# Optimization experiments

Hardware: AMD Instinct MI355X
Metric: run time of the kernel (lower is better)

The kernel has to match this reference:

```python
import jax, jax.numpy as jnp
import numpy as np

B, S, V, D, H, L, FF = 2, 1024, 32000, 512, 8, 4, 2048
DK = D // H
WIN, GLOB = 128, 16
EPS = 1e-5


def setup_inputs() -> dict:
    key = jax.random.key(0)
    ks = jax.random.split(key, 12)
    def rn(k, shape, s=0.02):
        return jax.random.normal(k, shape, jnp.float32) * s
    ln2 = jnp.stack([jnp.ones((L, 2, D)), jnp.zeros((L, 2, D))], axis=2)   # [L, 2 norms, (scale,bias), D]
    ln3 = jnp.stack([jnp.ones((L, 3, D)), jnp.zeros((L, 3, D))], axis=2)   # [L, 3 norms, (scale,bias), D]
    fln = jnp.stack([jnp.ones((D,)), jnp.zeros((D,))], axis=0)             # [(scale,bias), D]
    return {
        "src": jax.random.randint(ks[0], (B, S), 0, V),
        "tgt": jax.random.randint(ks[1], (B, S), 0, V),
        "enc_embed": rn(ks[2], (V, D)),
        "dec_embed": rn(ks[3], (V, D)),
        "enc_attn_w": rn(ks[4], (L, 4, D, D)),   # q,k,v,o projections
        "enc_attn_b": jnp.zeros((L, 4, D)),
        "enc_ln": ln2,
        "enc_ffn_w1": rn(ks[5], (L, D, FF)),
        "enc_ffn_b1": jnp.zeros((L, FF)),
        "enc_ffn_w2": rn(ks[6], (L, FF, D)),
        "enc_ffn_b2": jnp.zeros((L, D)),
        "enc_final_ln": fln,
        "dec_attn_w": rn(ks[7], (L, 8, D, D)),   # self q,k,v,o then cross q,k,v,o
        "dec_attn_b": jnp.zeros((L, 8, D)),
        "dec_ln": ln3,
        "dec_ffn_w1": rn(ks[8], (L, D, FF)),
        "dec_ffn_b1": jnp.zeros((L, FF)),
        "dec_ffn_w2": rn(ks[9], (L, FF, D)),
        "dec_ffn_b2": jnp.zeros((L, D)),
        "dec_final_ln": fln,
        "out_w": rn(ks[10], (D, V)),
        "out_b": jnp.zeros((V,)),
    }


def _ln(x, p):
    m = jnp.mean(x, -1, keepdims=True)
    v = jnp.var(x, -1, keepdims=True)
    return p[0] * (x - m) * jax.lax.rsqrt(v + EPS) + p[1]


def _rope(x):
    # x: [B, H, S, DK]; half-split rotary embedding
    half = DK // 2
    pos = jnp.arange(x.shape[2], dtype=jnp.float32)
    inv = 1.0 / (10000.0 ** (jnp.arange(half, dtype=jnp.float32) / half))
    ang = pos[:, None] * inv[None, :]                   # [S, half]
    c, s = jnp.cos(ang), jnp.sin(ang)
    x1, x2 = x[..., :half], x[..., half:]
    return jnp.concatenate([x1 * c - x2 * s, x1 * s + x2 * c], axis=-1)


def _mask(n, causal):
    # local sliding window + global tokens, optional causal
    i = jnp.arange(n)[:, None]
    j = jnp.arange(n)[None, :]
    allowed = jnp.abs(i - j) <= WIN
    allowed = allowed | (i < GLOB) | (j < GLOB)
    if causal:
        allowed = allowed & (j <= i)
    return allowed


def _attn(q_in, k_in, v_in, w, b, causal):
    # w: [4, D, D] (q,k,v,o), b: [4, D]
    def heads(x, idx):
        y = x @ w[idx] + b[idx]
        return y.reshape(x.shape[0], x.shape[1], H, DK).transpose(0, 2, 1, 3)  # [B,H,S,DK]
    Q, K, Vh = heads(q_in, 0), heads(k_in, 1), heads(v_in, 2)
    Q, K = _rope(Q), _rope(K)
    scores = jnp.einsum('bhqd,bhkd->bhqk', Q, K) / np.sqrt(DK).astype(np.float32)
    scores = jnp.where(_mask(q_in.shape[1], causal)[None, None], scores, -1e9)
    A = jax.nn.softmax(scores, axis=-1)
    o = jnp.einsum('bhqk,bhkd->bhqd', A, Vh).transpose(0, 2, 1, 3).reshape(q_in.shape[0], q_in.shape[1], D)
    return o @ w[3] + b[3]


def _ffn(x, w1, b1, w2, b2):
    return jax.nn.gelu(x @ w1 + b1) @ w2 + b2


def _forward(src, tgt, enc_embed, dec_embed, enc_attn_w, enc_attn_b, enc_ln,
             enc_ffn_w1, enc_ffn_b1, enc_ffn_w2, enc_ffn_b2, enc_final_ln,
             dec_attn_w, dec_attn_b, dec_ln, dec_ffn_w1, dec_ffn_b1,
             dec_ffn_w2, dec_ffn_b2, dec_final_ln, out_w, out_b):
    sqrt_d = np.sqrt(D).astype(np.float32)
    # encoder
    x = enc_embed[src] * sqrt_d
    for l in range(L):
        n = _ln(x, enc_ln[l, 0])
        x = x + _attn(n, n, n, enc_attn_w[l], enc_attn_b[l], False)
        n = _ln(x, enc_ln[l, 1])
        x = x + _ffn(n, enc_ffn_w1[l], enc_ffn_b1[l], enc_ffn_w2[l], enc_ffn_b2[l])
    mem = _ln(x, enc_final_ln)
    # decoder
    y = dec_embed[tgt] * sqrt_d
    for l in range(L):
        n = _ln(y, dec_ln[l, 0])
        y = y + _attn(n, n, n, dec_attn_w[l, :4], dec_attn_b[l, :4], True)
        n = _ln(y, dec_ln[l, 1])
        y = y + _attn(n, mem, mem, dec_attn_w[l, 4:], dec_attn_b[l, 4:], False)
        n = _ln(y, dec_ln[l, 2])
        y = y + _ffn(n, dec_ffn_w1[l], dec_ffn_b1[l], dec_ffn_w2[l], dec_ffn_b2[l])
    y = _ln(y, dec_final_ln)
    return y @ out_w + out_b


def reference(src, tgt, enc_embed, dec_embed, enc_attn_w, enc_attn_b, enc_ln,
              enc_ffn_w1, enc_ffn_b1, enc_ffn_w2, enc_ffn_b2, enc_final_ln,
              dec_attn_w, dec_attn_b, dec_ln, dec_ffn_w1, dec_ffn_b1,
              dec_ffn_w2, dec_ffn_b2, dec_final_ln, out_w, out_b):
    return _forward(src, tgt, enc_embed, dec_embed, enc_attn_w, enc_attn_b, enc_ln,
                    enc_ffn_w1, enc_ffn_b1, enc_ffn_w2, enc_ffn_b2, enc_final_ln,
                    dec_attn_w, dec_attn_b, dec_ln, dec_ffn_w1, dec_ffn_b1,
                    dec_ffn_w2, dec_ffn_b2, dec_final_ln, out_w, out_b)
```

## Files before the change

kernel.cpp:

```cpp
#include <hip/hip_runtime.h>
#include <cstdint>
#include <cstddef>

#define S_LEN 1024
#define DM 512
#define NHEAD 8
#define HDIM 64
#define NLAYER 4
#define FFD 2048
#define VOC 32000
#define WINSZ 128
#define GLOBSZ 16

using half8 = __attribute__((ext_vector_type(8))) _Float16;
using f32x4 = __attribute__((ext_vector_type(4))) float;

static __device__ __forceinline__ f32x4 mfma16(half8 a, half8 b, f32x4 c) {
  return __builtin_amdgcn_mfma_f32_16x16x32_f16(a, b, c, 0, 0, 0);
}

typedef __attribute__((address_space(1))) const void gvoid;
typedef __attribute__((address_space(3))) void lvoid;
static __device__ __forceinline__ void gload16(const void* g, void* l) {
  __builtin_amdgcn_global_load_lds((gvoid*)g, (lvoid*)l, 16, 0, 0);
}
template <int N>
static __device__ __forceinline__ void waitv() {
  asm volatile("s_waitcnt vmcnt(%0)" :: "i"(N) : "memory");
}

__global__ __launch_bounds__(256) void transpose_k(const float* __restrict__ in,
                                                   _Float16* __restrict__ out,
                                                   int R, int C)
{
  __shared__ float t[32][33];
  const float* ip = in + (size_t)blockIdx.z * R * C;
  _Float16* op = out + (size_t)blockIdx.z * R * C;
  int c0 = blockIdx.x * 32, r0 = blockIdx.y * 32;
  int tx = threadIdx.x & 31, ty = threadIdx.x >> 5;
#pragma unroll
  for (int i = 0; i < 32; i += 8)
    t[ty + i][tx] = ip[(size_t)(r0 + ty + i) * C + c0 + tx];
  __syncthreads();
#pragma unroll
  for (int i = 0; i < 32; i += 8)
    op[(size_t)(c0 + ty + i) * R + r0 + tx] = (_Float16)t[tx][ty + i];
}

__global__ __launch_bounds__(256) void embed2_k(const int* __restrict__ src,
                                                const int* __restrict__ tgt,
                                                const float* __restrict__ enc_embed,
                                                const float* __restrict__ dec_embed,
                                                const float* __restrict__ enc_ln0,
                                                const float* __restrict__ dec_ln0,
                                                float* __restrict__ xbuf,
                                                float* __restrict__ ybuf,
                                                _Float16* __restrict__ nbuf,
                                                _Float16* __restrict__ nbuf2)
{
  int which = blockIdx.y;
  const int* ids = which ? tgt : src;
  const float* emb = which ? dec_embed : enc_embed;
  const float* gamma = which ? dec_ln0 : enc_ln0;
  const float* beta = gamma + 512;
  float* xout = which ? ybuf : xbuf;
  _Float16* nout = which ? nbuf2 : nbuf;

  int row = blockIdx.x * 4 + (threadIdx.x >> 6);
  int lane = threadIdx.x & 63;
  const float* er = emb + (size_t)ids[row] * DM + lane * 8;
  float4 v0 = *(const float4*)er;
  float4 v1 = *(const float4*)(er + 4);
  float vals[8] = {v0.x, v0.y, v0.z, v0.w, v1.x, v1.y, v1.z, v1.w};
  float s = 0.f, ss = 0.f;
#pragma unroll
  for (int j = 0; j < 8; ++j) {
    vals[j] *= 22.627416997969522f;
    s += vals[j]; ss += vals[j] * vals[j];
  }
#pragma unroll
  for (int m = 1; m < 64; m <<= 1) { s += __shfl_xor(s, m); ss += __shfl_xor(ss, m); }
  float mean = s * (1.f / 512.f);
  float var = ss * (1.f / 512.f) - mean * mean;
  float rstd = rsqrtf(var + 1e-5f);
  float* xr = xout + (size_t)row * DM + lane * 8;
  _Float16* orow = nout + (size_t)row * DM + lane * 8;
  const float* gp = gamma + lane * 8;
  const float* bp = beta + lane * 8;
#pragma unroll
  for (int j = 0; j < 8; ++j) {
    xr[j] = vals[j];
    orow[j] = (_Float16)(gp[j] * (vals[j] - mean) * rstd + bp[j]);
  }
}

__global__ __launch_bounds__(256) void ln_k(const float* __restrict__ x,
                                            const float* __restrict__ gamma,
                                            const float* __restrict__ beta,
                                            _Float16* __restrict__ outp)
{
  int row = blockIdx.x * 4 + (threadIdx.x >> 6);
  int lane = threadIdx.x & 63;
  const float* xr = x + (size_t)row * DM + lane * 8;
  float4 v0 = *(const float4*)xr;
  float4 v1 = *(const float4*)(xr + 4);
  float vals[8] = {v0.x, v0.y, v0.z, v0.w, v1.x, v1.y, v1.z, v1.w};
  float s = 0.f, ss = 0.f;
#pragma unroll
  for (int j = 0; j < 8; ++j) { s += vals[j]; ss += vals[j] * vals[j]; }
#pragma unroll
  for (int m = 1; m < 64; m <<= 1) { s += __shfl_xor(s, m); ss += __shfl_xor(ss, m); }
  float mean = s * (1.f / 512.f);
  float var = ss * (1.f / 512.f) - mean * mean;
  float rstd = rsqrtf(var + 1e-5f);
  _Float16* orow = outp + (size_t)row * DM + lane * 8;
  const float* gp = gamma + lane * 8;
  const float* bp = beta + lane * 8;
#pragma unroll
  for (int j = 0; j < 8; ++j)
    orow[j] = (_Float16)(gp[j] * (vals[j] - mean) * rstd + bp[j]);
}

template <int BM, int BN, int EPI, int MODE>
__global__ __launch_bounds__(256) void gemm_k(const _Float16* __restrict__ A,
                                              const _Float16* __restrict__ B,
                                              const float* __restrict__ bias,
                                              const float* __restrict__ resid,
                                              void* __restrict__ Cout,
                                              _Float16* __restrict__ vtout,
                                              int M, int N, int K)
{
  constexpr bool WIDE = (BN >= 64);
  constexpr int WAVE_M = WIDE ? BM / 4 : BM / 2;
  constexpr int FMW = WAVE_M / 16;
  constexpr int FNW = WIDE ? BN / 16 : BN / 32;
  constexpr int LPS = BM / 32 + BN / 32;
  static_assert(MODE == 0 || (WIDE && BN == 64), "rope modes need 64-col waves");

  __shared__ __align__(16) _Float16 As[3][BM * 64];
  __shared__ __align__(16) _Float16 Bs[3][BN * 64];
  const int tid = threadIdx.x;
  const int lane = tid & 63, wid = tid >> 6;
  const int g = lane >> 4, ql = lane & 15;
  const int bm = blockIdx.x * BM, bn = blockIdx.y * BN;
  const int wm = WIDE ? wid * WAVE_M : (wid >> 1) * WAVE_M;
  const int wn = WIDE ? 0 : (wid & 1) * (BN / 2);

  const _Float16* Bp;
  if constexpr (MODE == 2) {
    int srcrow0 = ((bn >> 10) * 8 + 5 + ((bn >> 9) & 1)) * 512 + (bn & 511);
    Bp = B + (size_t)srcrow0 * K;
  } else {
    Bp = B + (size_t)bn * K;
  }

  f32x4 acc[FMW][FNW];
#pragma unroll
  for (int a = 0; a < FMW; ++a)
#pragma unroll
    for (int b = 0; b < FNW; ++b) acc[a][b] = f32x4{0.f, 0.f, 0.f, 0.f};

  auto stage = [&](int buf, int kt) {
#pragma unroll
    for (int r = 0; r < BM / 32; ++r) {
      int off = r * 4096 + tid * 16;
      int row = off >> 7, slot = (off >> 4) & 7;
      gload16(A + (size_t)(bm + row) * K + kt + ((slot ^ (row & 7)) << 3),
              (char*)&As[buf][0] + r * 4096 + wid * 1024);
    }
#pragma unroll
    for (int r = 0; r < BN / 32; ++r) {
      int off = r * 4096 + tid * 16;
      int row = off >> 7, slot = (off >> 4) & 7;
      gload16(Bp + (size_t)row * K + kt + ((slot ^ (row & 7)) << 3),
              (char*)&Bs[buf][0] + r * 4096 + wid * 1024);
    }
  };

  auto compute = [&](int cur) {
#pragma unroll
    for (int kk = 0; kk < 2; ++kk) {
      half8 af[FMW], bf[FNW];
#pragma unroll
      for (int a = 0; a < FMW; ++a) {
        int row = wm + a * 16 + ql;
        af[a] = *(const half8*)((const char*)&As[cur][0] + row * 128 + (((kk * 4 + g) ^ (row & 7)) << 4));
      }
#pragma unroll
      for (int b = 0; b < FNW; ++b) {
        int row = wn + b * 16 + ql;
        bf[b] = *(const half8*)((const char*)&Bs[cur][0] + row * 128 + (((kk * 4 + g) ^ (row & 7)) << 4));
      }
#pragma unroll
      for (int a = 0; a < FMW; ++a)
#pragma unroll
        for (int b = 0; b < FNW; ++b) acc[a][b] = mfma16(af[a], bf[b], acc[a][b]);
    }
  };

  const int nk = K >> 6;
  stage(0, 0);
  stage(1, 64);
  for (int t = 0; t < nk; ++t) {
    if (t + 1 < nk) waitv<LPS>(); else waitv<0>();
    __builtin_amdgcn_s_barrier();
    __builtin_amdgcn_sched_barrier(0);
    compute(t % 3);
    if (t + 2 < nk) stage((t + 2) % 3, (t + 2) << 6);
  }

#pragma unroll
  for (int a = 0; a < FMW; ++a) {
    const int row0 = bm + wm + a * 16 + g * 4;
    float v[FNW][4];
#pragma unroll
    for (int b2 = 0; b2 < FNW; ++b2) {
      int col = bn + wn + b2 * 16 + ql;
      float bv;
      if constexpr (MODE == 2) {
        int bcol = ((col >> 10) * 8 + 5 + ((col >> 9) & 1)) * 512 + (col & 511);
        bv = bias[bcol];
      } else {
        bv = bias[col];
      }
#pragma unroll
      for (int r = 0; r < 4; ++r) v[b2][r] = acc[a][b2][r] + bv;
    }
    if constexpr (MODE != 0) {
      const int seg = bn >> 9;
      bool dorope = (MODE == 3) || (MODE == 1 && seg < 2) ||
                    (MODE == 2 && ((bn >> 9) & 1) == 0);
      if (dorope) {
        const float scale = (MODE == 3 || (MODE == 1 && seg == 0)) ? 0.125f : 1.0f;
#pragma unroll
        for (int b2 = 0; b2 < 2; ++b2) {
          int d = b2 * 16 + ql;
          float inv = __expf(-(float)d * 0.28782313662425574f);
#pragma unroll
          for (int r = 0; r < 4; ++r) {
            float sp = (float)((row0 & 1023) + r);
            float sn, cs; __sincosf(sp * inv, &sn, &cs);
            float x1 = v[b2][r], x2 = v[b2 + 2][r];
            v[b2][r]     = (x1 * cs - x2 * sn) * scale;
            v[b2 + 2][r] = (x1 * sn + x2 * cs) * scale;
          }
        }
      }
    }
#pragma unroll
    for (int b2 = 0; b2 < FNW; ++b2) {
      int col = bn + wn + b2 * 16 + ql;
      if constexpr (MODE == 1) {
        if (col < 1024) {
#pragma unroll
          for (int r = 0; r < 4; ++r)
            ((_Float16*)Cout)[(size_t)(row0 + r) * 1024 + col] = (_Float16)v[b2][r];
        } else {
          int rowidx = ((row0 >> 10) << 9) + (col - 1024);
          union { _Float16 h[4]; uint2 u; } pk;
#pragma unroll
          for (int r = 0; r < 4; ++r) pk.h[r] = (_Float16)v[b2][r];
          *(uint2*)&vtout[((size_t)rowidx << 10) + (row0 & 1023)] = pk.u;
        }
      } else if constexpr (MODE == 2) {
        if ((col & 1023) < 512) {
#pragma unroll
          for (int r = 0; r < 4; ++r)
            ((_Float16*)Cout)[(size_t)(row0 + r) * 2048 + ((col >> 10) << 9) + (col & 511)] = (_Float16)v[b2][r];
        } else {
          int rowidx = (col & ~1023) + ((row0 >> 10) << 9) + (col & 511);
          union { _Float16 h[4]; uint2 u; } pk;
#pragma unroll
          for (int r = 0; r < 4; ++r) pk.h[r] = (_Float16)v[b2][r];
          *(uint2*)&vtout[((size_t)rowidx << 10) + (row0 & 1023)] = pk.u;
        }
      } else {
#pragma unroll
        for (int r = 0; r < 4; ++r) {
          float x = v[b2][r];
          if constexpr (EPI == 1) {
            float u = x;
            x = u / (1.f + __expf(-1.5957691216057308f * (u + 0.044715f * u * u * u)));
          }
          if constexpr (EPI == 2) x += resid[(size_t)(row0 + r) * N + col];
          if constexpr (EPI == 0 || EPI == 1)
            ((_Float16*)Cout)[(size_t)(row0 + r) * N + col] = (_Float16)x;
          else
            ((float*)Cout)[(size_t)(row0 + r) * N + col] = x;
        }
      }
    }
  }
}

template <bool CAUSAL>
__global__ __launch_bounds__(256) void attn_k(const _Float16* __restrict__ qb, int qs, int qoff,
                                              const _Float16* __restrict__ kb, int ks, int koff,
                                              const _Float16* __restrict__ vt,
                                              _Float16* __restrict__ out)
{
  __shared__ _Float16 plds[4][16 * 40];
  const int bh = blockIdx.y, b = bh >> 3, h = bh & 7;
  const int wid = threadIdx.x >> 6, lane = threadIdx.x & 63;
  const int g = lane >> 4, ql = lane & 15;
  const int q0 = blockIdx.x * 64 + wid * 16;
  const size_t rb = (size_t)b * S_LEN;

  half8 qf0, qf1;
  {
    const _Float16* qp = qb + (rb + q0 + ql) * qs + qoff + h * HDIM + g * 8;
    qf0 = *(const half8*)qp;
    qf1 = *(const half8*)(qp + 32);
  }
  float mrun[4] = {-1e30f, -1e30f, -1e30f, -1e30f};
  float srun[4] = {0.f, 0.f, 0.f, 0.f};
  f32x4 oacc[4];
#pragma unroll
  for (int c = 0; c < 4; ++c) oacc[c] = f32x4{0.f, 0.f, 0.f, 0.f};

  const _Float16* vbase = vt + (((size_t)(b * 512 + h * HDIM)) << 10);
  _Float16* pw = plds[wid];

  auto proc = [&](int k0) {
    const _Float16* kp = kb + (rb + k0 + ql) * ks + koff + h * HDIM + g * 8;
    half8 kf00 = *(const half8*)kp;
    half8 kf01 = *(const half8*)(kp + 32);
    half8 kf10 = *(const half8*)(kp + (size_t)16 * ks);
    half8 kf11 = *(const half8*)(kp + (size_t)16 * ks + 32);

    f32x4 s0 = f32x4{0.f, 0.f, 0.f, 0.f};
    f32x4 s1 = f32x4{0.f, 0.f, 0.f, 0.f};
    s0 = mfma16(qf0, kf00, s0); s0 = mfma16(qf1, kf01, s0);
    s1 = mfma16(qf0, kf10, s1); s1 = mfma16(qf1, kf11, s1);

    float p0[4], p1[4];
#pragma unroll
    for (int r = 0; r < 4; ++r) {
      int i = q0 + 4 * g + r;
      int j0 = k0 + ql, j1 = j0 + 16;
      float a0 = s0[r], a1 = s1[r];
      int d0 = i - j0, d1 = i - j1;
      bool ok0 = (d0 <= WINSZ && d0 >= -WINSZ) || (i < GLOBSZ) || (j0 < GLOBSZ);
      bool ok1 = (d1 <= WINSZ && d1 >= -WINSZ) || (i < GLOBSZ) || (j1 < GLOBSZ);
      if (CAUSAL) { ok0 = ok0 && (j0 <= i); ok1 = ok1 && (j1 <= i); }
      a0 = ok0 ? a0 : -1e9f;
      a1 = ok1 ? a1 : -1e9f;
      float mx = fmaxf(a0, a1);
      mx = fmaxf(mx, __shfl_xor(mx, 1));
      mx = fmaxf(mx, __shfl_xor(mx, 2));
      mx = fmaxf(mx, __shfl_xor(mx, 4));
      mx = fmaxf(mx, __shfl_xor(mx, 8));
      float mnew = fmaxf(mrun[r], mx);
      float alpha = __expf(mrun[r] - mnew);
      float e0 = __expf(a0 - mnew), e1 = __expf(a1 - mnew);
      float ps = e0 + e1;
      ps += __shfl_xor(ps, 1);
      ps += __shfl_xor(ps, 2);
      ps += __shfl_xor(ps, 4);
      ps += __shfl_xor(ps, 8);
      srun[r] = srun[r] * alpha + ps;
      mrun[r] = mnew;
#pragma unroll
      for (int c = 0; c < 4; ++c) oacc[c][r] *= alpha;
      p0[r] = e0; p1[r] = e1;
    }
#pragma unroll
    for (int r = 0; r < 4; ++r) {
      pw[(4 * g + r) * 40 + ql] = (_Float16)p0[r];
      pw[(4 * g + r) * 40 + 16 + ql] = (_Float16)p1[r];
    }
    half8 pa = *(const half8*)&pw[ql * 40 + g * 8];
#pragma unroll
    for (int c = 0; c < 4; ++c) {
      half8 vf = *(const half8*)(vbase + (((size_t)(16 * c + ql)) << 10) + k0 + 8 * g);
      oacc[c] = mfma16(pa, vf, oacc[c]);
    }
  };

  const int kend = CAUSAL ? (q0 + 16) : S_LEN;
  int lo = 0, hi = kend;
  if (q0 >= GLOBSZ) {
    lo = (q0 - WINSZ) & ~31;
    if (lo < 0) lo = 0;
    if (!CAUSAL) {
      int h2 = q0 + 16 + WINSZ;
      hi = (h2 < kend) ? h2 : kend;
    }
  }
  if (lo > 0) proc(0);
  for (int k0 = lo; k0 < hi; k0 += 32) proc(k0);

#pragma unroll
  for (int c = 0; c < 4; ++c)
#pragma unroll
    for (int r = 0; r < 4; ++r) {
      float val = oacc[c][r] / srun[r];
      out[(rb + q0 + 4 * g + r) * DM + h * HDIM + 16 * c + ql] = (_Float16)val;
    }
}

extern "C" void kernel_launch(void* const* d_in, const int* in_sizes, int n_in,
                              void* d_out, int out_size, void* d_ws, size_t ws_size,
                              hipStream_t stream)
{
  const int*   src         = (const int*)d_in[0];
  const int*   tgt         = (const int*)d_in[1];
  const float* enc_embed   = (const float*)d_in[2];
  const float* dec_embed   = (const float*)d_in[3];
  const float* enc_attn_w  = (const float*)d_in[4];
  const float* enc_attn_b  = (const float*)d_in[5];
  const float* enc_ln      = (const float*)d_in[6];
  const float* enc_ffn_w1  = (const float*)d_in[7];
  const float* enc_ffn_b1  = (const float*)d_in[8];
  const float* enc_ffn_w2  = (const float*)d_in[9];
  const float* enc_ffn_b2  = (const float*)d_in[10];
  const float* enc_fln     = (const float*)d_in[11];
  const float* dec_attn_w  = (const float*)d_in[12];
  const float* dec_attn_b  = (const float*)d_in[13];
  const float* dec_ln      = (const float*)d_in[14];
  const float* dec_ffn_w1  = (const float*)d_in[15];
  const float* dec_ffn_b1  = (const float*)d_in[16];
  const float* dec_ffn_w2  = (const float*)d_in[17];
  const float* dec_ffn_b2  = (const float*)d_in[18];
  const float* dec_fln     = (const float*)d_in[19];
  const float* out_w       = (const float*)d_in[20];
  const float* out_b       = (const float*)d_in[21];
  float* logits = (float*)d_out;

  char* wsp = (char*)d_ws;
  size_t off = 0;
  auto alloc = [&](size_t bytes) -> void* {
    void* p = wsp + off;
    off += (bytes + 255) & ~(size_t)255;
    return p;
  };
  _Float16* enc_attn_wt = (_Float16*)alloc((size_t)16 * 512 * 512 * 2);
  _Float16* dec_attn_wt = (_Float16*)alloc((size_t)32 * 512 * 512 * 2);
  _Float16* e_ffn1_wt   = (_Float16*)alloc((size_t)4 * 2048 * 512 * 2);
  _Float16* e_ffn2_wt   = (_Float16*)alloc((size_t)4 * 2048 * 512 * 2);
  _Float16* d_ffn1_wt   = (_Float16*)alloc((size_t)4 * 2048 * 512 * 2);
  _Float16* d_ffn2_wt   = (_Float16*)alloc((size_t)4 * 2048 * 512 * 2);
  _Float16* out_wt      = (_Float16*)alloc((size_t)VOC * 512 * 2);
  float*    xbuf        = (float*)alloc((size_t)2048 * 512 * 4);
  float*    ybuf        = (float*)alloc((size_t)2048 * 512 * 4);
  _Float16* nbuf        = (_Float16*)alloc((size_t)2048 * 512 * 2);
  _Float16* nbuf2       = (_Float16*)alloc((size_t)2048 * 512 * 2);
  _Float16* qkvb        = (_Float16*)alloc((size_t)2048 * 1024 * 2);
  _Float16* aob         = (_Float16*)alloc((size_t)2048 * 512 * 2);
  _Float16* hbuf        = (_Float16*)alloc((size_t)2048 * 2048 * 2);
  _Float16* memb        = (_Float16*)alloc((size_t)2048 * 512 * 2);
  _Float16* cqb         = (_Float16*)alloc((size_t)2048 * 512 * 2);
  _Float16* ckvb        = (_Float16*)alloc((size_t)2048 * 2048 * 2);
  _Float16* vts         = (_Float16*)alloc((size_t)2 * 512 * 1024 * 2);
  _Float16* vtc         = (_Float16*)alloc((size_t)8 * 512 * 1024 * 2);

  transpose_k<<<dim3(16, 16, 16), 256, 0, stream>>>(enc_attn_w, enc_attn_wt, 512, 512);
  transpose_k<<<dim3(16, 16, 32), 256, 0, stream>>>(dec_attn_w, dec_attn_wt, 512, 512);
  transpose_k<<<dim3(64, 16, 4), 256, 0, stream>>>(enc_ffn_w1, e_ffn1_wt, 512, 2048);
  transpose_k<<<dim3(16, 64, 4), 256, 0, stream>>>(enc_ffn_w2, e_ffn2_wt, 2048, 512);
  transpose_k<<<dim3(64, 16, 4), 256, 0, stream>>>(dec_ffn_w1, d_ffn1_wt, 512, 2048);
  transpose_k<<<dim3(16, 64, 4), 256, 0, stream>>>(dec_ffn_w2, d_ffn2_wt, 2048, 512);
  transpose_k<<<dim3(1000, 16, 1), 256, 0, stream>>>(out_w, out_wt, 512, VOC);

  embed2_k<<<dim3(512, 2), 256, 0, stream>>>(src, tgt, enc_embed, dec_embed,
                                             enc_ln, dec_ln, xbuf, ybuf, nbuf, nbuf2);

  for (int l = 0; l < NLAYER; ++l) {
    const float* g0 = enc_ln + ((size_t)(l * 2 + 0) * 2 + 0) * 512;
    if (l > 0) ln_k<<<512, 256, 0, stream>>>(xbuf, g0, g0 + 512, nbuf);
    gemm_k<64, 64, 0, 1><<<dim3(32, 24), 256, 0, stream>>>(
        nbuf, enc_attn_wt + (size_t)l * 4 * 262144,
        enc_attn_b + (size_t)l * 4 * 512, nullptr, qkvb, vts, 2048, 1536, 512);
    attn_k<false><<<dim3(16, 16), 256, 0, stream>>>(qkvb, 1024, 0, qkvb, 1024, 512, vts, aob);
    gemm_k<64, 32, 2, 0><<<dim3(32, 16), 256, 0, stream>>>(
        aob, enc_attn_wt + (size_t)(l * 4 + 3) * 262144,
        enc_attn_b + (size_t)(l * 4 + 3) * 512, xbuf, xbuf, nullptr, 2048, 512, 512);
    const float* g1 = enc_ln + ((size_t)(l * 2 + 1) * 2 + 0) * 512;
    ln_k<<<512, 256, 0, stream>>>(xbuf, g1, g1 + 512, nbuf);
    gemm_k<64, 64, 1, 0><<<dim3(32, 32), 256, 0, stream>>>(
        nbuf, e_ffn1_wt + (size_t)l * 2048 * 512,
        enc_ffn_b1 + (size_t)l * 2048, nullptr, hbuf, nullptr, 2048, 2048, 512);
    gemm_k<64, 32, 2, 0><<<dim3(32, 16), 256, 0, stream>>>(
        hbuf, e_ffn2_wt + (size_t)l * 512 * 2048,
        enc_ffn_b2 + (size_t)l * 512, xbuf, xbuf, nullptr, 2048, 512, 2048);
  }
  ln_k<<<512, 256, 0, stream>>>(xbuf, enc_fln, enc_fln + 512, memb);

  gemm_k<64, 64, 0, 2><<<dim3(32, 64), 256, 0, stream>>>(
      memb, dec_attn_wt, dec_attn_b, nullptr, ckvb, vtc, 2048, 4096, 512);

  for (int l = 0; l < NLAYER; ++l) {
    const float* g0 = dec_ln + ((size_t)(l * 3 + 0) * 2 + 0) * 512;
    const _Float16* dn = (l == 0) ? nbuf2 : nbuf;
    if (l > 0) ln_k<<<512, 256, 0, stream>>>(ybuf, g0, g0 + 512, nbuf);
    gemm_k<64, 64, 0, 1><<<dim3(32, 24), 256, 0, stream>>>(
        dn, dec_attn_wt + (size_t)l * 8 * 262144,
        dec_attn_b + (size_t)l * 8 * 512, nullptr, qkvb, vts, 2048, 1536, 512);
    attn_k<true><<<dim3(16, 16), 256, 0, stream>>>(qkvb, 1024, 0, qkvb, 1024, 512, vts, aob);
    gemm_k<64, 32, 2, 0><<<dim3(32, 16), 256, 0, stream>>>(
        aob, dec_attn_wt + (size_t)(l * 8 + 3) * 262144,
        dec_attn_b + (size_t)(l * 8 + 3) * 512, ybuf, ybuf, nullptr, 2048, 512, 512);
    const float* g1 = dec_ln + ((size_t)(l * 3 + 1) * 2 + 0) * 512;
    ln_k<<<512, 256, 0, stream>>>(ybuf, g1, g1 + 512, nbuf);
    gemm_k<64, 64, 0, 3><<<dim3(32, 8), 256, 0, stream>>>(
        nbuf, dec_attn_wt + (size_t)(l * 8 + 4) * 262144,
        dec_attn_b + (size_t)(l * 8 + 4) * 512, nullptr, cqb, nullptr, 2048, 512, 512);
    attn_k<false><<<dim3(16, 16), 256, 0, stream>>>(cqb, 512, 0, ckvb, 2048, l * 512,
                                                    vtc + ((size_t)l << 20), aob);
    gemm_k<64, 32, 2, 0><<<dim3(32, 16), 256, 0, stream>>>(
        aob, dec_attn_wt + (size_t)(l * 8 + 7) * 262144,
        dec_attn_b + (size_t)(l * 8 + 7) * 512, ybuf, ybuf, nullptr, 2048, 512, 512);
    const float* g2 = dec_ln + ((size_t)(l * 3 + 2) * 2 + 0) * 512;
    ln_k<<<512, 256, 0, stream>>>(ybuf, g2, g2 + 512, nbuf);
    gemm_k<64, 64, 1, 0><<<dim3(32, 32), 256, 0, stream>>>(
        nbuf, d_ffn1_wt + (size_t)l * 2048 * 512,
        dec_ffn_b1 + (size_t)l * 2048, nullptr, hbuf, nullptr, 2048, 2048, 512);
    gemm_k<64, 32, 2, 0><<<dim3(32, 16), 256, 0, stream>>>(
        hbuf, d_ffn2_wt + (size_t)l * 512 * 2048,
        dec_ffn_b2 + (size_t)l * 512, ybuf, ybuf, nullptr, 2048, 512, 2048);
  }

  ln_k<<<512, 256, 0, stream>>>(ybuf, dec_fln, dec_fln + 512, nbuf);
  gemm_k<128, 64, 3, 0><<<dim3(16, 500), 256, 0, stream>>>(
      nbuf, out_wt, out_b, nullptr, logits, nullptr, 2048, VOC, 512);
}
```

Before: 1.061 ms.

## Remap GEMM blocks across XCDs, prefetch before compute, widen residual tiles

The GEMM kernel remaps its linear block id so that consecutive tiles land on the same XCD chiplet, which is meant to improve L2 reuse of shared A/B panels. The next-stage global-to-LDS load is now issued before the MFMA compute instead of after it, to overlap more. The residual GEMMs move from 64x32 tiles (512 blocks) to 64x64 tiles (256 blocks), dropping the narrow-wave path. The logits output uses nontemporal stores. These trade fewer blocks (less parallelism on 256 CUs) and a possible LDS hazard from issuing the load early against better reuse and overlap.

```diff
diff --git a/kernel.cpp b/kernel.cpp
--- a/kernel.cpp
+++ b/kernel.cpp
@@ -130,21 +130,26 @@
                                               _Float16* __restrict__ vtout,
                                               int M, int N, int K)
 {
-  constexpr bool WIDE = (BN >= 64);
-  constexpr int WAVE_M = WIDE ? BM / 4 : BM / 2;
+  constexpr int WAVE_M = BM / 4;
   constexpr int FMW = WAVE_M / 16;
-  constexpr int FNW = WIDE ? BN / 16 : BN / 32;
+  constexpr int FNW = BN / 16;
   constexpr int LPS = BM / 32 + BN / 32;
-  static_assert(MODE == 0 || (WIDE && BN == 64), "rope modes need 64-col waves");
+  static_assert(BN == 64 || MODE == 0, "rope modes need 64-col waves");
 
   __shared__ __align__(16) _Float16 As[3][BM * 64];
   __shared__ __align__(16) _Float16 Bs[3][BN * 64];
   const int tid = threadIdx.x;
   const int lane = tid & 63, wid = tid >> 6;
   const int g = lane >> 4, ql = lane & 15;
-  const int bm = blockIdx.x * BM, bn = blockIdx.y * BN;
-  const int wm = WIDE ? wid * WAVE_M : (wid >> 1) * WAVE_M;
-  const int wn = WIDE ? 0 : (wid & 1) * (BN / 2);
+
+  const int gx = gridDim.x;
+  const int nwg = gx * gridDim.y;
+  const int orig = blockIdx.y * gx + blockIdx.x;
+  const int q = nwg >> 3, r = nwg & 7;
+  const int xcd = orig & 7, rest = orig >> 3;
+  const int id = (xcd < r ? xcd * (q + 1) : r * (q + 1) + (xcd - r) * q) + rest;
+  const int bm = (id % gx) * BM, bn = (id / gx) * BN;
+  const int wm = wid * WAVE_M, wn = 0;
 
   const _Float16* Bp;
   if constexpr (MODE == 2) {
@@ -162,18 +167,18 @@
 
   auto stage = [&](int buf, int kt) {
 #pragma unroll
-    for (int r = 0; r < BM / 32; ++r) {
-      int off = r * 4096 + tid * 16;
+    for (int r2 = 0; r2 < BM / 32; ++r2) {
+      int off = r2 * 4096 + tid * 16;
       int row = off >> 7, slot = (off >> 4) & 7;
       gload16(A + (size_t)(bm + row) * K + kt + ((slot ^ (row & 7)) << 3),
-              (char*)&As[buf][0] + r * 4096 + wid * 1024);
-    }
-#pragma unroll
-    for (int r = 0; r < BN / 32; ++r) {
-      int off = r * 4096 + tid * 16;
+              (char*)&As[buf][0] + r2 * 4096 + wid * 1024);
+    }
+#pragma unroll
+    for (int r2 = 0; r2 < BN / 32; ++r2) {
+      int off = r2 * 4096 + tid * 16;
       int row = off >> 7, slot = (off >> 4) & 7;
       gload16(Bp + (size_t)row * K + kt + ((slot ^ (row & 7)) << 3),
-              (char*)&Bs[buf][0] + r * 4096 + wid * 1024);
+              (char*)&Bs[buf][0] + r2 * 4096 + wid * 1024);
     }
   };
 
@@ -205,8 +210,8 @@
     if (t + 1 < nk) waitv<LPS>(); else waitv<0>();
     __builtin_amdgcn_s_barrier();
     __builtin_amdgcn_sched_barrier(0);
+    if (t + 2 < nk) stage((t + 2) % 3, (t + 2) << 6);
     compute(t % 3);
-    if (t + 2 < nk) stage((t + 2) % 3, (t + 2) << 6);
   }
 
 #pragma unroll
@@ -224,7 +229,7 @@
         bv = bias[col];
       }
 #pragma unroll
-      for (int r = 0; r < 4; ++r) v[b2][r] = acc[a][b2][r] + bv;
+      for (int r2 = 0; r2 < 4; ++r2) v[b2][r2] = acc[a][b2][r2] + bv;
     }
     if constexpr (MODE != 0) {
       const int seg = bn >> 9;
@@ -237,12 +242,12 @@
           int d = b2 * 16 + ql;
           float inv = __expf(-(float)d * 0.28782313662425574f);
 #pragma unroll
-          for (int r = 0; r < 4; ++r) {
-            float sp = (float)((row0 & 1023) + r);
+          for (int r2 = 0; r2 < 4; ++r2) {
+            float sp = (float)((row0 & 1023) + r2);
             float sn, cs; __sincosf(sp * inv, &sn, &cs);
-            float x1 = v[b2][r], x2 = v[b2 + 2][r];
-            v[b2][r]     = (x1 * cs - x2 * sn) * scale;
-            v[b2 + 2][r] = (x1 * sn + x2 * cs) * scale;
+            float x1 = v[b2][r2], x2 = v[b2 + 2][r2];
+            v[b2][r2]     = (x1 * cs - x2 * sn) * scale;
+            v[b2 + 2][r2] = (x1 * sn + x2 * cs) * scale;
           }
         }
       }
@@ -253,40 +258,42 @@
       if constexpr (MODE == 1) {
         if (col < 1024) {
 #pragma unroll
-          for (int r = 0; r < 4; ++r)
-            ((_Float16*)Cout)[(size_t)(row0 + r) * 1024 + col] = (_Float16)v[b2][r];
+          for (int r2 = 0; r2 < 4; ++r2)
+            ((_Float16*)Cout)[(size_t)(row0 + r2) * 1024 + col] = (_Float16)v[b2][r2];
         } else {
           int rowidx = ((row0 >> 10) << 9) + (col - 1024);
           union { _Float16 h[4]; uint2 u; } pk;
 #pragma unroll
-          for (int r = 0; r < 4; ++r) pk.h[r] = (_Float16)v[b2][r];
+          for (int r2 = 0; r2 < 4; ++r2) pk.h[r2] = (_Float16)v[b2][r2];
           *(uint2*)&vtout[((size_t)rowidx << 10) + (row0 & 1023)] = pk.u;
         }
       } else if constexpr (MODE == 2) {
         if ((col & 1023) < 512) {
 #pragma unroll
-          for (int r = 0; r < 4; ++r)
-            ((_Float16*)Cout)[(size_t)(row0 + r) * 2048 + ((col >> 10) << 9) + (col & 511)] = (_Float16)v[b2][r];
+          for (int r2 = 0; r2 < 4; ++r2)
+            ((_Float16*)Cout)[(size_t)(row0 + r2) * 2048 + ((col >> 10) << 9) + (col & 511)] = (_Float16)v[b2][r2];
         } else {
           int rowidx = (col & ~1023) + ((row0 >> 10) << 9) + (col & 511);
           union { _Float16 h[4]; uint2 u; } pk;
 #pragma unroll
-          for (int r = 0; r < 4; ++r) pk.h[r] = (_Float16)v[b2][r];
+          for (int r2 = 0; r2 < 4; ++r2) pk.h[r2] = (_Float16)v[b2][r2];
           *(uint2*)&vtout[((size_t)rowidx << 10) + (row0 & 1023)] = pk.u;
         }
       } else {
 #pragma unroll
-        for (int r = 0; r < 4; ++r) {
-          float x = v[b2][r];
+        for (int r2 = 0; r2 < 4; ++r2) {
+          float x = v[b2][r2];
           if constexpr (EPI == 1) {
             float u = x;
             x = u / (1.f + __expf(-1.5957691216057308f * (u + 0.044715f * u * u * u)));
           }
-          if constexpr (EPI == 2) x += resid[(size_t)(row0 + r) * N + col];
+          if constexpr (EPI == 2) x += resid[(size_t)(row0 + r2) * N + col];
           if constexpr (EPI == 0 || EPI == 1)
-            ((_Float16*)Cout)[(size_t)(row0 + r) * N + col] = (_Float16)x;
+            ((_Float16*)Cout)[(size_t)(row0 + r2) * N + col] = (_Float16)x;
+          else if constexpr (EPI == 2)
+            ((float*)Cout)[(size_t)(row0 + r2) * N + col] = x;
           else
-            ((float*)Cout)[(size_t)(row0 + r) * N + col] = x;
+            __builtin_nontemporal_store(x, &((float*)Cout)[(size_t)(row0 + r2) * N + col]);
         }
       }
     }
@@ -472,7 +479,7 @@
         nbuf, enc_attn_wt + (size_t)l * 4 * 262144,
         enc_attn_b + (size_t)l * 4 * 512, nullptr, qkvb, vts, 2048, 1536, 512);
     attn_k<false><<<dim3(16, 16), 256, 0, stream>>>(qkvb, 1024, 0, qkvb, 1024, 512, vts, aob);
-    gemm_k<64, 32, 2, 0><<<dim3(32, 16), 256, 0, stream>>>(
+    gemm_k<64, 64, 2, 0><<<dim3(32, 8), 256, 0, stream>>>(
         aob, enc_attn_wt + (size_t)(l * 4 + 3) * 262144,
         enc_attn_b + (size_t)(l * 4 + 3) * 512, xbuf, xbuf, nullptr, 2048, 512, 512);
     const float* g1 = enc_ln + ((size_t)(l * 2 + 1) * 2 + 0) * 512;
@@ -480,7 +487,7 @@
     gemm_k<64, 64, 1, 0><<<dim3(32, 32), 256, 0, stream>>>(
         nbuf, e_ffn1_wt + (size_t)l * 2048 * 512,
         enc_ffn_b1 + (size_t)l * 2048, nullptr, hbuf, nullptr, 2048, 2048, 512);
-    gemm_k<64, 32, 2, 0><<<dim3(32, 16), 256, 0, stream>>>(
+    gemm_k<64, 64, 2, 0><<<dim3(32, 8), 256, 0, stream>>>(
         hbuf, e_ffn2_wt + (size_t)l * 512 * 2048,
         enc_ffn_b2 + (size_t)l * 512, xbuf, xbuf, nullptr, 2048, 512, 2048);
   }
@@ -497,7 +504,7 @@
         dn, dec_attn_wt + (size_t)l * 8 * 262144,
         dec_attn_b + (size_t)l * 8 * 512, nullptr, qkvb, vts, 2048, 1536, 512);
     attn_k<true><<<dim3(16, 16), 256, 0, stream>>>(qkvb, 1024, 0, qkvb, 1024, 512, vts, aob);
-    gemm_k<64, 32, 2, 0><<<dim3(32, 16), 256, 0, stream>>>(
+    gemm_k<64, 64, 2, 0><<<dim3(32, 8), 256, 0, stream>>>(
         aob, dec_attn_wt + (size_t)(l * 8 + 3) * 262144,
         dec_attn_b + (size_t)(l * 8 + 3) * 512, ybuf, ybuf, nullptr, 2048, 512, 512);
     const float* g1 = dec_ln + ((size_t)(l * 3 + 1) * 2 + 0) * 512;
@@ -507,7 +514,7 @@
         dec_attn_b + (size_t)(l * 8 + 4) * 512, nullptr, cqb, nullptr, 2048, 512, 512);
     attn_k<false><<<dim3(16, 16), 256, 0, stream>>>(cqb, 512, 0, ckvb, 2048, l * 512,
                                                     vtc + ((size_t)l << 20), aob);
-    gemm_k<64, 32, 2, 0><<<dim3(32, 16), 256, 0, stream>>>(
+    gemm_k<64, 64, 2, 0><<<dim3(32, 8), 256, 0, stream>>>(
         aob, dec_attn_wt + (size_t)(l * 8 + 7) * 262144,
         dec_attn_b + (size_t)(l * 8 + 7) * 512, ybuf, ybuf, nullptr, 2048, 512, 512);
     const float* g2 = dec_ln + ((size_t)(l * 3 + 2) * 2 + 0) * 512;
@@ -515,7 +522,7 @@
     gemm_k<64, 64, 1, 0><<<dim3(32, 32), 256, 0, stream>>>(
         nbuf, d_ffn1_wt + (size_t)l * 2048 * 512,
         dec_ffn_b1 + (size_t)l * 2048, nullptr, hbuf, nullptr, 2048, 2048, 512);
-    gemm_k<64, 32, 2, 0><<<dim3(32, 16), 256, 0, stream>>>(
+    gemm_k<64, 64, 2, 0><<<dim3(32, 8), 256, 0, stream>>>(
         hbuf, d_ffn2_wt + (size_t)l * 512 * 2048,
         dec_ffn_b2 + (size_t)l * 512, ybuf, ybuf, nullptr, 2048, 512, 2048);
   }
```

After: 1.114 ms. +5.0%, slower.
